# Optimization experiments

Hardware: AMD Instinct MI355X
Metric: run time of the kernel (lower is better)

## Reference

```python
import jax, jax.numpy as jnp
import numpy as np

T, N, F_IND, F_MAC = 250, 4000, 46, 178
H = 64
F_IN = F_IND + F_MAC  # dense-net input = firm chars + tiled macro = 224


def setup_inputs() -> dict:
    key = jax.random.key(0)
    ks = jax.random.split(key, 9)
    macro_features = jax.random.normal(ks[0], (1, T, F_MAC), jnp.float32)
    individual_features = jax.random.normal(ks[1], (1, T, N, F_IND), jnp.float32)
    masks = jnp.ones((1, T, N, 1), dtype=bool)
    returns_tensor = jax.random.normal(ks[2], (1, T, N, 1), jnp.float32) * 0.05
    W1 = jax.random.normal(ks[3], (F_IN, H), jnp.float32) / np.sqrt(F_IN).astype(np.float32)
    b1 = jnp.zeros((H,), jnp.float32)
    W2 = jax.random.normal(ks[4], (H, H), jnp.float32) / np.sqrt(H).astype(np.float32)
    b2 = jnp.zeros((H,), jnp.float32)
    W3 = jax.random.normal(ks[5], (H, 1), jnp.float32) / np.sqrt(H).astype(np.float32)
    b3 = jnp.zeros((1,), jnp.float32)
    return {"macro_features": macro_features, "individual_features": individual_features,
            "masks": masks, "returns_tensor": returns_tensor,
            "W1": W1, "b1": b1, "W2": W2, "b2": b2, "W3": W3, "b3": b3}


def reference(macro_features, individual_features, masks, returns_tensor, W1, b1, W2, b2, W3, b3):
    B, Tt, Nn, _ = individual_features.shape
    # tile macro state over assets and concat with firm characteristics -> [1,T,N,F_IN]
    mac = jnp.broadcast_to(macro_features[:, :, None, :], (B, Tt, Nn, macro_features.shape[-1]))
    dense_inputs = jnp.concatenate([individual_features, mac], axis=-1)
    mf = masks.astype(dense_inputs.dtype)  # [1,T,N,1]
    # dense net: 2 relu hidden layers + linear head, output_size=1 (SDF weight per firm-month)
    h = jax.nn.relu(dense_inputs @ W1 + b1)
    h = jax.nn.relu(h @ W2 + b2)
    weights = (h @ W3 + b3) * mf  # zero out masked entries (mask is all-ones -> static shape)
    # weighted returns and per-time segment sum (== torch.split + per-segment torch.sum)
    weighted_returns = returns_tensor * weights * mf
    num_val_per_time = jnp.sum(mf[0, :, :, 0], axis=1)  # [T]
    sum_per_time = jnp.sum(weighted_returns[0, :, :, 0], axis=1)  # [T]
    # normalize_w = True
    sum_per_time = sum_per_time / num_val_per_time * jnp.mean(num_val_per_time)
    sdf = (sum_per_time + 1.0)[:, None]  # [T,1]
    weights_flat = weights.reshape(1, Tt * Nn, 1)  # matches masked_select layout (all-true mask)
    return sdf, weights_flat
```

## Files before the change

### kernel.cpp

```cpp
#include <hip/hip_runtime.h>

#define T_DIM 250
#define N_DIM 4000
#define F_IND 46
#define F_MAC 178
#define H_DIM 64

typedef __bf16         bf16x8  __attribute__((ext_vector_type(8)));
typedef float          f32x4   __attribute__((ext_vector_type(4)));
typedef unsigned short ushort8 __attribute__((ext_vector_type(8)));
typedef float          f32x4a8 __attribute__((ext_vector_type(4), aligned(8)));

union FragU { ushort8 u; bf16x8 b; unsigned w[4]; };
union BF2   { unsigned u; __bf16 h[2]; };

__device__ __forceinline__ unsigned short f2bf(float f) {
    unsigned u = __float_as_uint(f);
    return (unsigned short)((u + 0x7fffu + ((u >> 16) & 1u)) >> 16);
}
__device__ __forceinline__ unsigned packbf2(float lo, float hi) {
    BF2 p; p.h[0] = (__bf16)lo; p.h[1] = (__bf16)hi; return p.u;
}

__global__ __launch_bounds__(256)
void prep_kernel(const float* __restrict__ mac,
                 const float* __restrict__ W1,
                 const float* __restrict__ b1,
                 const float* __restrict__ W2,
                 unsigned short* __restrict__ Wb1,
                 unsigned short* __restrict__ Wb2,
                 float* __restrict__ Mproj,
                 float* __restrict__ sdf)
{
    const int b = blockIdx.x;
    const int tid = threadIdx.x;
    if (b < 2) {
        const float* W = (b == 0) ? W1 : W2;
        unsigned short* dst = (b == 0) ? Wb1 : Wb2;
        const int kmax = (b == 0) ? F_IND : H_DIM;
        for (int idx = tid; idx < 4096; idx += 256) {
            int j  = idx & 7;
            int L  = (idx >> 3) & 63;
            int rt = (idx >> 9) & 3;
            int s  = idx >> 11;
            int k  = s * 32 + ((L >> 4) * 8) + j;
            int c  = rt * 16 + (L & 15);
            float v = (k < kmax) ? W[k * H_DIM + c] : 0.0f;
            dst[idx] = f2bf(v);
        }
    } else {
        __shared__ float red[4][H_DIM];
        const int t  = b - 2;
        const int j  = tid & 63;
        const int kc = tid >> 6;
        const int k0 = kc * 45;
        const int k1 = (k0 + 45 < F_MAC) ? k0 + 45 : F_MAC;
        float acc = (kc == 0) ? b1[j] : 0.0f;
        const float* mrow = mac + t * F_MAC;
        for (int k = k0; k < k1; ++k)
            acc = fmaf(mrow[k], W1[(F_IND + k) * H_DIM + j], acc);
        red[kc][j] = acc;
        __syncthreads();
        if (tid < 64) {
            Mproj[t * H_DIM + j] = red[0][j] + red[1][j] + red[2][j] + red[3][j];
            if (tid == 0) sdf[t] = 1.0f;
        }
    }
}

__global__ __launch_bounds__(256)
void mlp_mfma(const float* __restrict__ ind,
              const float* __restrict__ ret,
              const unsigned short* __restrict__ Wb1,
              const unsigned short* __restrict__ Wb2,
              const float* __restrict__ Mproj,
              const float* __restrict__ b2,
              const float* __restrict__ W3,
              const float* __restrict__ b3,
              float* __restrict__ out_w,
              float* __restrict__ sdf)
{
    __shared__ unsigned Hsh[256 * 32];

    const int tid  = threadIdx.x;
    const int lane = tid & 63;
    const int w    = tid >> 6;
    const int q    = lane >> 4;
    const int m    = lane & 15;
    const int m7   = m & 7;
    const int t    = blockIdx.y;
    const int nbase = blockIdx.x * 2048;
    const int w64  = w * 64;
    const int rbase = w64;

    FragU a1[8];
    #pragma unroll
    for (int f = 0; f < 8; ++f)
        a1[f].u = *(const ushort8*)(Wb1 + (f * 64 + lane) * 8);
    f32x4 mp[4];
    #pragma unroll
    for (int rt = 0; rt < 4; ++rt)
        mp[rt] = *(const f32x4*)(Mproj + t * H_DIM + rt * 16 + q * 4);

    const float* xrw = ind + ((size_t)t * N_DIM + nbase + w64 + m) * F_IND;
    const float* rp  = ret + (size_t)t * N_DIM + nbase + w64 + lane;
    const int CTS = 16 * F_IND;

    f32x4a8 xa[4], xb[4], ya[4], yb[4];
    float retv;
    const f32x4a8 z4 = {};

    auto issue = [&](int ni) {
        const float* xr = xrw + (size_t)ni * (256 * F_IND);
        const int nwv = nbase + ni * 256 + w64;
        const bool fullw = (nwv + 64 <= N_DIM);
        if (fullw) {
            #pragma unroll
            for (int ct = 0; ct < 4; ++ct) {
                const float* p = xr + ct * CTS + q * 8;
                xa[ct] = *(const f32x4a8*)(p);
                xb[ct] = *(const f32x4a8*)(p + 4);
            }
        } else {
            #pragma unroll
            for (int ct = 0; ct < 4; ++ct) {
                const float* p = xr + ct * CTS + q * 8;
                if ((nwv + ct * 16 + m) < N_DIM) {
                    xa[ct] = *(const f32x4a8*)(p);
                    xb[ct] = *(const f32x4a8*)(p + 4);
                } else { xa[ct] = z4; xb[ct] = z4; }
            }
        }
        #pragma unroll
        for (int ct = 0; ct < 4; ++ct) { ya[ct] = z4; yb[ct] = z4; }
        if (q == 0) {
            #pragma unroll
            for (int ct = 0; ct < 4; ++ct)
                if (fullw || (nwv + ct * 16 + m) < N_DIM) {
                    ya[ct] = *(const f32x4a8*)(xr + ct * CTS + 32);
                    yb[ct] = *(const f32x4a8*)(xr + ct * CTS + 36);
                }
        } else if (q == 1) {
            #pragma unroll
            for (int ct = 0; ct < 4; ++ct)
                if (fullw || (nwv + ct * 16 + m) < N_DIM) {
                    ya[ct] = *(const f32x4a8*)(xr + ct * CTS + 40);
                    float2 z = *(const float2*)(xr + ct * CTS + 44);
                    yb[ct][0] = z.x; yb[ct][1] = z.y;
                }
        }
        retv = 0.0f;
        if (nwv + lane < N_DIM) retv = rp[ni * 256];
    };

    issue(0);

    #pragma unroll 1
    for (int ni = 0; ni < 8; ++ni) {
        FragU xf[4], yf[4];
        #pragma unroll
        for (int ct = 0; ct < 4; ++ct)
            #pragma unroll
            for (int i = 0; i < 4; ++i) {
                xf[ct].b[i]     = (__bf16)xa[ct][i];
                xf[ct].b[i + 4] = (__bf16)xb[ct][i];
                yf[ct].b[i]     = (__bf16)ya[ct][i];
                yf[ct].b[i + 4] = (__bf16)yb[ct][i];
            }
        const float retc = retv;
        const int nwv   = nbase + ni * 256 + w64;
        const int nlane = nwv + lane;

        if (ni < 7) issue(ni + 1);

        f32x4 acc[4][4];
        #pragma unroll
        for (int rt = 0; rt < 4; ++rt)
            #pragma unroll
            for (int ct = 0; ct < 4; ++ct)
                acc[rt][ct] = mp[rt];

        #pragma unroll
        for (int rt = 0; rt < 4; ++rt)
            #pragma unroll
            for (int ct = 0; ct < 4; ++ct)
                acc[rt][ct] = __builtin_amdgcn_mfma_f32_16x16x32_bf16(
                    a1[rt].b, xf[ct].b, acc[rt][ct], 0, 0, 0);
        #pragma unroll
        for (int rt = 0; rt < 4; ++rt)
            #pragma unroll
            for (int ct = 0; ct < 4; ++ct)
                acc[rt][ct] = __builtin_amdgcn_mfma_f32_16x16x32_bf16(
                    a1[4 + rt].b, yf[ct].b, acc[rt][ct], 0, 0, 0);

        FragU a2[2][4];
        #pragma unroll
        for (int s = 0; s < 2; ++s)
            #pragma unroll
            for (int rt = 0; rt < 4; ++rt)
                a2[s][rt].u = *(const ushort8*)(Wb2 + ((s * 4 + rt) * 64 + lane) * 8);
        f32x4 bb2[4], w3[4];
        #pragma unroll
        for (int rt = 0; rt < 4; ++rt) {
            bb2[rt] = *(const f32x4*)(b2 + rt * 16 + q * 4);
            w3[rt]  = *(const f32x4*)(W3 + rt * 16 + q * 4);
        }
        const float b3s = b3[0];

        #pragma unroll
        for (int rt = 0; rt < 4; ++rt)
            #pragma unroll
            for (int ct = 0; ct < 4; ++ct) {
                int sl = ct * 16 + m;
                unsigned lo = packbf2(fmaxf(acc[rt][ct][0], 0.0f),
                                      fmaxf(acc[rt][ct][1], 0.0f));
                unsigned hi = packbf2(fmaxf(acc[rt][ct][2], 0.0f),
                                      fmaxf(acc[rt][ct][3], 0.0f));
                int phys = ((rt * 2 + (q >> 1)) ^ m7) * 4 + (q & 1) * 2;
                uint2 v; v.x = lo; v.y = hi;
                *(uint2*)(Hsh + (rbase + sl) * 32 + phys) = v;
            }

        #pragma unroll
        for (int rt = 0; rt < 4; ++rt)
            #pragma unroll
            for (int ct = 0; ct < 4; ++ct)
                acc[rt][ct] = bb2[rt];

        #pragma unroll
        for (int s = 0; s < 2; ++s) {
            FragU hf[4];
            #pragma unroll
            for (int ct = 0; ct < 4; ++ct) {
                int sl  = ct * 16 + m;
                int blk = (s * 4 + q) ^ m7;
                hf[ct].u = *(const ushort8*)(Hsh + (rbase + sl) * 32 + blk * 4);
            }
            #pragma unroll
            for (int rt = 0; rt < 4; ++rt)
                #pragma unroll
                for (int ct = 0; ct < 4; ++ct)
                    acc[rt][ct] = __builtin_amdgcn_mfma_f32_16x16x32_bf16(
                        a2[s][rt].b, hf[ct].b, acc[rt][ct], 0, 0, 0);
        }

        float pq[4];
        #pragma unroll
        for (int ct = 0; ct < 4; ++ct) {
            float p = 0.0f;
            #pragma unroll
            for (int rt = 0; rt < 4; ++rt)
                #pragma unroll
                for (int r = 0; r < 4; ++r)
                    p = fmaf(fmaxf(acc[rt][ct][r], 0.0f), w3[rt][r], p);
            p += __shfl_xor(p, 16, 64);
            p += __shfl_xor(p, 32, 64);
            pq[ct] = p;
        }
        float wv = (q == 0) ? pq[0] : (q == 1) ? pq[1] : (q == 2) ? pq[2] : pq[3];
        wv += b3s;

        float contrib = 0.0f;
        if (nlane < N_DIM) {
            out_w[(size_t)t * N_DIM + nlane] = wv;
            contrib = retc * wv;
        }
        #pragma unroll
        for (int off = 32; off > 0; off >>= 1)
            contrib += __shfl_down(contrib, off, 64);
        if (lane == 0) atomicAdd(&sdf[t], contrib);
    }
}

extern "C" void kernel_launch(void* const* d_in, const int* in_sizes, int n_in,
                              void* d_out, int out_size, void* d_ws, size_t ws_size,
                              hipStream_t stream) {
    (void)in_sizes; (void)n_in; (void)out_size; (void)ws_size;

    const float* mac = (const float*)d_in[0];
    const float* ind = (const float*)d_in[1];
    const float* ret = (const float*)d_in[3];
    const float* W1  = (const float*)d_in[4];
    const float* b1  = (const float*)d_in[5];
    const float* W2  = (const float*)d_in[6];
    const float* b2  = (const float*)d_in[7];
    const float* W3  = (const float*)d_in[8];
    const float* b3  = (const float*)d_in[9];

    float* sdf   = (float*)d_out;
    float* out_w = (float*)d_out + T_DIM;

    unsigned short* Wb1 = (unsigned short*)d_ws;
    unsigned short* Wb2 = Wb1 + 4096;
    float* Mproj = (float*)((char*)d_ws + 16384);

    prep_kernel<<<dim3(252), 256, 0, stream>>>(mac, W1, b1, W2, Wb1, Wb2, Mproj, sdf);

    dim3 grid(2, T_DIM);
    mlp_mfma<<<grid, 256, 0, stream>>>(ind, ret, Wb1, Wb2, Mproj, b2, W3, b3,
                                       out_w, sdf);
}
```

Measured before the change: 311.4 us.

## Split MLP kernel into many small single-pass blocks for higher occupancy

Replaces the 2-block-per-timestep grid with 32 blocks per timestep. Each wave now processes 32 assets in one pass instead of looping over 8 software-pipelined chunks of 64. This exposes far more parallelism across CUs and halves shared memory and register use, adding launch bounds for 4 blocks per CU. In exchange it drops the prefetch pipelining, reloads weight fragments per wave, and issues more atomic adds to the per-time sdf accumulator.

```diff
diff --git a/kernel.cpp b/kernel.cpp
--- a/kernel.cpp
+++ b/kernel.cpp
@@ -68,7 +68,7 @@
     }
 }
 
-__global__ __launch_bounds__(256)
+__global__ __launch_bounds__(256, 4)
 void mlp_mfma(const float* __restrict__ ind,
               const float* __restrict__ ret,
               const unsigned short* __restrict__ Wb1,
@@ -80,7 +80,7 @@
               float* __restrict__ out_w,
               float* __restrict__ sdf)
 {
-    __shared__ unsigned Hsh[256 * 32];
+    __shared__ unsigned Hsh[128 * 32];
 
     const int tid  = threadIdx.x;
     const int lane = tid & 63;
@@ -89,164 +89,133 @@
     const int m    = lane & 15;
     const int m7   = m & 7;
     const int t    = blockIdx.y;
-    const int nbase = blockIdx.x * 2048;
-    const int w64  = w * 64;
-    const int rbase = w64;
+    const int nwv  = blockIdx.x * 128 + w * 32;
+
+    if (nwv >= N_DIM) return;
+    const int rbase = w * 32;
+
+    const float retv = (lane < 32) ? ret[(size_t)t * N_DIM + nwv + lane] : 0.0f;
+
+    const float* xr = ind + ((size_t)t * N_DIM + (nwv + m)) * F_IND;
+    const int CTS = 16 * F_IND;
+
+    f32x4a8 xa[2], xb[2];
+    #pragma unroll
+    for (int ct = 0; ct < 2; ++ct) {
+        const float* p = xr + ct * CTS + q * 8;
+        xa[ct] = *(const f32x4a8*)(p);
+        xb[ct] = *(const f32x4a8*)(p + 4);
+    }
+    f32x4a8 ya[2] = {}, yb[2] = {};
+    if (q == 0) {
+        #pragma unroll
+        for (int ct = 0; ct < 2; ++ct) {
+            ya[ct] = *(const f32x4a8*)(xr + ct * CTS + 32);
+            yb[ct] = *(const f32x4a8*)(xr + ct * CTS + 36);
+        }
+    } else if (q == 1) {
+        #pragma unroll
+        for (int ct = 0; ct < 2; ++ct) {
+            ya[ct] = *(const f32x4a8*)(xr + ct * CTS + 40);
+            float2 z = *(const float2*)(xr + ct * CTS + 44);
+            yb[ct][0] = z.x; yb[ct][1] = z.y;
+        }
+    }
 
     FragU a1[8];
     #pragma unroll
     for (int f = 0; f < 8; ++f)
         a1[f].u = *(const ushort8*)(Wb1 + (f * 64 + lane) * 8);
-    f32x4 mp[4];
-    #pragma unroll
-    for (int rt = 0; rt < 4; ++rt)
-        mp[rt] = *(const f32x4*)(Mproj + t * H_DIM + rt * 16 + q * 4);
-
-    const float* xrw = ind + ((size_t)t * N_DIM + nbase + w64 + m) * F_IND;
-    const float* rp  = ret + (size_t)t * N_DIM + nbase + w64 + lane;
-    const int CTS = 16 * F_IND;
-
-    f32x4a8 xa[4], xb[4], ya[4], yb[4];
-    float retv;
-    const f32x4a8 z4 = {};
-
-    auto issue = [&](int ni) {
-        const float* xr = xrw + (size_t)ni * (256 * F_IND);
-        const int nwv = nbase + ni * 256 + w64;
-        const bool fullw = (nwv + 64 <= N_DIM);
-        if (fullw) {
-            #pragma unroll
-            for (int ct = 0; ct < 4; ++ct) {
-                const float* p = xr + ct * CTS + q * 8;
-                xa[ct] = *(const f32x4a8*)(p);
-                xb[ct] = *(const f32x4a8*)(p + 4);
-            }
-        } else {
-            #pragma unroll
-            for (int ct = 0; ct < 4; ++ct) {
-                const float* p = xr + ct * CTS + q * 8;
-                if ((nwv + ct * 16 + m) < N_DIM) {
-                    xa[ct] = *(const f32x4a8*)(p);
-                    xb[ct] = *(const f32x4a8*)(p + 4);
-                } else { xa[ct] = z4; xb[ct] = z4; }
-            }
-        }
-        #pragma unroll
-        for (int ct = 0; ct < 4; ++ct) { ya[ct] = z4; yb[ct] = z4; }
-        if (q == 0) {
-            #pragma unroll
-            for (int ct = 0; ct < 4; ++ct)
-                if (fullw || (nwv + ct * 16 + m) < N_DIM) {
-                    ya[ct] = *(const f32x4a8*)(xr + ct * CTS + 32);
-                    yb[ct] = *(const f32x4a8*)(xr + ct * CTS + 36);
-                }
-        } else if (q == 1) {
-            #pragma unroll
-            for (int ct = 0; ct < 4; ++ct)
-                if (fullw || (nwv + ct * 16 + m) < N_DIM) {
-                    ya[ct] = *(const f32x4a8*)(xr + ct * CTS + 40);
-                    float2 z = *(const float2*)(xr + ct * CTS + 44);
-                    yb[ct][0] = z.x; yb[ct][1] = z.y;
-                }
-        }
-        retv = 0.0f;
-        if (nwv + lane < N_DIM) retv = rp[ni * 256];
-    };
-
-    issue(0);
-
-    #pragma unroll 1
-    for (int ni = 0; ni < 8; ++ni) {
-        FragU xf[4], yf[4];
-        #pragma unroll
-        for (int ct = 0; ct < 4; ++ct)
-            #pragma unroll
-            for (int i = 0; i < 4; ++i) {
-                xf[ct].b[i]     = (__bf16)xa[ct][i];
-                xf[ct].b[i + 4] = (__bf16)xb[ct][i];
-                yf[ct].b[i]     = (__bf16)ya[ct][i];
-                yf[ct].b[i + 4] = (__bf16)yb[ct][i];
-            }
-        const float retc = retv;
-        const int nwv   = nbase + ni * 256 + w64;
-        const int nlane = nwv + lane;
-
-        if (ni < 7) issue(ni + 1);
-
-        f32x4 acc[4][4];
+
+    f32x4 acc[4][2];
+    #pragma unroll
+    for (int rt = 0; rt < 4; ++rt) {
+        f32x4 mpv = *(const f32x4*)(Mproj + t * H_DIM + rt * 16 + q * 4);
+        acc[rt][0] = mpv;
+        acc[rt][1] = mpv;
+    }
+
+    FragU xf[2], yf[2];
+    #pragma unroll
+    for (int ct = 0; ct < 2; ++ct)
+        #pragma unroll
+        for (int i = 0; i < 4; ++i) {
+            xf[ct].b[i]     = (__bf16)xa[ct][i];
+            xf[ct].b[i + 4] = (__bf16)xb[ct][i];
+            yf[ct].b[i]     = (__bf16)ya[ct][i];
+            yf[ct].b[i + 4] = (__bf16)yb[ct][i];
+        }
+
+    #pragma unroll
+    for (int rt = 0; rt < 4; ++rt)
+        #pragma unroll
+        for (int ct = 0; ct < 2; ++ct)
+            acc[rt][ct] = __builtin_amdgcn_mfma_f32_16x16x32_bf16(
+                a1[rt].b, xf[ct].b, acc[rt][ct], 0, 0, 0);
+    #pragma unroll
+    for (int rt = 0; rt < 4; ++rt)
+        #pragma unroll
+        for (int ct = 0; ct < 2; ++ct)
+            acc[rt][ct] = __builtin_amdgcn_mfma_f32_16x16x32_bf16(
+                a1[4 + rt].b, yf[ct].b, acc[rt][ct], 0, 0, 0);
+
+    FragU a2[8];
+    #pragma unroll
+    for (int f = 0; f < 8; ++f)
+        a2[f].u = *(const ushort8*)(Wb2 + (f * 64 + lane) * 8);
+    f32x4 bb2[4];
+    #pragma unroll
+    for (int rt = 0; rt < 4; ++rt)
+        bb2[rt] = *(const f32x4*)(b2 + rt * 16 + q * 4);
+
+    #pragma unroll
+    for (int rt = 0; rt < 4; ++rt)
+        #pragma unroll
+        for (int ct = 0; ct < 2; ++ct) {
+            int sl = ct * 16 + m;
+            unsigned lo = packbf2(fmaxf(acc[rt][ct][0], 0.0f),
+                                  fmaxf(acc[rt][ct][1], 0.0f));
+            unsigned hi = packbf2(fmaxf(acc[rt][ct][2], 0.0f),
+                                  fmaxf(acc[rt][ct][3], 0.0f));
+            int phys = ((rt * 2 + (q >> 1)) ^ m7) * 4 + (q & 1) * 2;
+            uint2 v; v.x = lo; v.y = hi;
+            *(uint2*)(Hsh + (rbase + sl) * 32 + phys) = v;
+        }
+
+    #pragma unroll
+    for (int rt = 0; rt < 4; ++rt)
+        #pragma unroll
+        for (int ct = 0; ct < 2; ++ct)
+            acc[rt][ct] = bb2[rt];
+
+    #pragma unroll
+    for (int s = 0; s < 2; ++s) {
+        FragU hf[2];
+        #pragma unroll
+        for (int ct = 0; ct < 2; ++ct) {
+            int sl  = ct * 16 + m;
+            int blk = (s * 4 + q) ^ m7;
+            hf[ct].u = *(const ushort8*)(Hsh + (rbase + sl) * 32 + blk * 4);
+        }
         #pragma unroll
         for (int rt = 0; rt < 4; ++rt)
             #pragma unroll
-            for (int ct = 0; ct < 4; ++ct)
-                acc[rt][ct] = mp[rt];
-
+            for (int ct = 0; ct < 2; ++ct)
+                acc[rt][ct] = __builtin_amdgcn_mfma_f32_16x16x32_bf16(
+                    a2[s * 4 + rt].b, hf[ct].b, acc[rt][ct], 0, 0, 0);
+    }
+
+    float wv;
+    {
+        f32x4 w3[4];
         #pragma unroll
         for (int rt = 0; rt < 4; ++rt)
-            #pragma unroll
-            for (int ct = 0; ct < 4; ++ct)
-                acc[rt][ct] = __builtin_amdgcn_mfma_f32_16x16x32_bf16(
-                    a1[rt].b, xf[ct].b, acc[rt][ct], 0, 0, 0);
-        #pragma unroll
-        for (int rt = 0; rt < 4; ++rt)
-            #pragma unroll
-            for (int ct = 0; ct < 4; ++ct)
-                acc[rt][ct] = __builtin_amdgcn_mfma_f32_16x16x32_bf16(
-                    a1[4 + rt].b, yf[ct].b, acc[rt][ct], 0, 0, 0);
-
-        FragU a2[2][4];
-        #pragma unroll
-        for (int s = 0; s < 2; ++s)
-            #pragma unroll
-            for (int rt = 0; rt < 4; ++rt)
-                a2[s][rt].u = *(const ushort8*)(Wb2 + ((s * 4 + rt) * 64 + lane) * 8);
-        f32x4 bb2[4], w3[4];
-        #pragma unroll
-        for (int rt = 0; rt < 4; ++rt) {
-            bb2[rt] = *(const f32x4*)(b2 + rt * 16 + q * 4);
-            w3[rt]  = *(const f32x4*)(W3 + rt * 16 + q * 4);
-        }
+            w3[rt] = *(const f32x4*)(W3 + rt * 16 + q * 4);
         const float b3s = b3[0];
 
-        #pragma unroll
-        for (int rt = 0; rt < 4; ++rt)
-            #pragma unroll
-            for (int ct = 0; ct < 4; ++ct) {
-                int sl = ct * 16 + m;
-                unsigned lo = packbf2(fmaxf(acc[rt][ct][0], 0.0f),
-                                      fmaxf(acc[rt][ct][1], 0.0f));
-                unsigned hi = packbf2(fmaxf(acc[rt][ct][2], 0.0f),
-                                      fmaxf(acc[rt][ct][3], 0.0f));
-                int phys = ((rt * 2 + (q >> 1)) ^ m7) * 4 + (q & 1) * 2;
-                uint2 v; v.x = lo; v.y = hi;
-                *(uint2*)(Hsh + (rbase + sl) * 32 + phys) = v;
-            }
-
-        #pragma unroll
-        for (int rt = 0; rt < 4; ++rt)
-            #pragma unroll
-            for (int ct = 0; ct < 4; ++ct)
-                acc[rt][ct] = bb2[rt];
-
-        #pragma unroll
-        for (int s = 0; s < 2; ++s) {
-            FragU hf[4];
-            #pragma unroll
-            for (int ct = 0; ct < 4; ++ct) {
-                int sl  = ct * 16 + m;
-                int blk = (s * 4 + q) ^ m7;
-                hf[ct].u = *(const ushort8*)(Hsh + (rbase + sl) * 32 + blk * 4);
-            }
-            #pragma unroll
-            for (int rt = 0; rt < 4; ++rt)
-                #pragma unroll
-                for (int ct = 0; ct < 4; ++ct)
-                    acc[rt][ct] = __builtin_amdgcn_mfma_f32_16x16x32_bf16(
-                        a2[s][rt].b, hf[ct].b, acc[rt][ct], 0, 0, 0);
-        }
-
-        float pq[4];
-        #pragma unroll
-        for (int ct = 0; ct < 4; ++ct) {
+        float pq[2];
+        #pragma unroll
+        for (int ct = 0; ct < 2; ++ct) {
             float p = 0.0f;
             #pragma unroll
             for (int rt = 0; rt < 4; ++rt)
@@ -257,19 +226,18 @@
             p += __shfl_xor(p, 32, 64);
             pq[ct] = p;
         }
-        float wv = (q == 0) ? pq[0] : (q == 1) ? pq[1] : (q == 2) ? pq[2] : pq[3];
-        wv += b3s;
-
-        float contrib = 0.0f;
-        if (nlane < N_DIM) {
-            out_w[(size_t)t * N_DIM + nlane] = wv;
-            contrib = retc * wv;
-        }
-        #pragma unroll
-        for (int off = 32; off > 0; off >>= 1)
-            contrib += __shfl_down(contrib, off, 64);
-        if (lane == 0) atomicAdd(&sdf[t], contrib);
-    }
+        wv = ((q & 1) ? pq[1] : pq[0]) + b3s;
+    }
+
+    float contrib = 0.0f;
+    if (lane < 32) {
+        out_w[(size_t)t * N_DIM + nwv + lane] = wv;
+        contrib = retv * wv;
+    }
+    #pragma unroll
+    for (int off = 16; off > 0; off >>= 1)
+        contrib += __shfl_down(contrib, off, 64);
+    if (lane == 0) atomicAdd(&sdf[t], contrib);
 }
 
 extern "C" void kernel_launch(void* const* d_in, const int* in_sizes, int n_in,
@@ -296,7 +264,7 @@
 
     prep_kernel<<<dim3(252), 256, 0, stream>>>(mac, W1, b1, W2, Wb1, Wb2, Mproj, sdf);
 
-    dim3 grid(2, T_DIM);
+    dim3 grid(32, T_DIM);
     mlp_mfma<<<grid, 256, 0, stream>>>(ind, ret, Wb1, Wb2, Mproj, b2, W3, b3,
                                        out_w, sdf);
 }
```

New measurement: 361.2 us. 16.0% more time.
